# Optimization experiments

Measured on AMD Instinct MI355X. Metric: run time of the kernel, lower is better.

## Reference

```python
import jax, jax.numpy as jnp
import numpy as np

B, L, D, H = 2, 2048, 2048, 16
DH = D // H  # 128


def setup_inputs() -> dict:
    key = jax.random.key(0)
    k1, k2 = jax.random.split(key)
    inputs = jax.random.normal(k1, (B, L, D), dtype=jnp.float32)
    # additive causal mask: 0 on/below diagonal, -inf above (matches typical usage)
    neg = jnp.finfo(jnp.float32).min
    causal = jnp.where(jnp.tril(jnp.ones((L, L), dtype=bool)), 0.0, neg)
    attn_mask = causal[None, None, :, :].astype(jnp.float32)
    # torch Linear(d, 3d, bias=False): y = x @ W.T; here W_qkv is stored as [d, 3d]
    W_qkv = jax.random.normal(k2, (D, 3 * D), dtype=jnp.float32) * (1.0 / np.sqrt(D))
    return {"inputs": inputs, "attn_mask": attn_mask, "W_qkv": W_qkv}


def reference(inputs, attn_mask, W_qkv):
    b, l, d = inputs.shape
    qkv = inputs @ W_qkv                       # [B, L, 3D]
    qkv = qkv.reshape(b, l, H, 3 * DH)         # [B, L, H, 3*dh]
    qkv = qkv.transpose(0, 2, 1, 3)            # [B, H, L, 3*dh]
    Q, K, V = jnp.split(qkv, 3, axis=-1)       # each [B, H, L, dh]
    scale = jnp.sqrt(jnp.float32(DH))
    scores = jnp.einsum("bhqd,bhkd->bhqk", Q, K) / scale
    scores = scores + attn_mask
    probs = jax.nn.softmax(scores, axis=-1)    # dropout is identity in eval / p=0
    out = jnp.einsum("bhqk,bhkd->bhqd", probs, V)
    out = out.transpose(0, 2, 1, 3).reshape(b, l, d)
    return out
```

## Files before the change

### kernel.cpp

```cpp
#include <hip/hip_runtime.h>

#define SEQL 2048
#define NHEAD 16
#define N3 6144
#define KDIM 2048

typedef __attribute__((ext_vector_type(8))) short bf16x8;
typedef __attribute__((ext_vector_type(4))) float f32x4;
typedef __attribute__((ext_vector_type(16))) float f32x16;
typedef __attribute__((ext_vector_type(4))) unsigned short us4;
typedef __attribute__((ext_vector_type(4))) float fl4;
typedef __attribute__((ext_vector_type(4))) unsigned int u32x4;

__device__ __forceinline__ unsigned short f2bf(float x) {
    unsigned u = __builtin_bit_cast(unsigned, x);
    u += 0x7fffu + ((u >> 16) & 1u);
    return (unsigned short)(u >> 16);
}

__device__ __forceinline__ void gload16(const void* g, void* l) {
    __builtin_amdgcn_global_load_lds(
        (const __attribute__((address_space(1))) unsigned int*)g,
        (__attribute__((address_space(3))) unsigned int*)l,
        16, 0, 0);
}

__device__ __forceinline__ unsigned cvtpk_bf16(float lo, float hi) {
    unsigned r;
    asm("v_cvt_pk_bf16_f32 %0, %1, %2" : "=v"(r) : "v"(lo), "v"(hi));
    return r;
}
__device__ __forceinline__ void plane32_swap(unsigned &a, unsigned &b) {
    asm("v_permlane32_swap_b32 %0, %1" : "+v"(a), "+v"(b));
}

__global__ __launch_bounds__(256) void k_convert_x(const float* __restrict__ in,
                                                   unsigned short* __restrict__ out) {
    int tid = blockIdx.x * 256 + threadIdx.x;
    const fl4* in4 = (const fl4*)in;
    us4* out4 = (us4*)out;
#pragma unroll
    for (int j = 0; j < 4; ++j) {
        int idx = tid + j * 524288;
        fl4 v = in4[idx];
        us4 o;
        o.x = f2bf(v.x); o.y = f2bf(v.y); o.z = f2bf(v.z); o.w = f2bf(v.w);
        out4[idx] = o;
    }
}

__global__ __launch_bounds__(256) void k_transpose_w(const float* __restrict__ W,
                                                     unsigned short* __restrict__ Wt) {
    __shared__ alignas(16) unsigned short Ts[64 * 68];
    int t = threadIdx.x;
    int n0 = blockIdx.x * 64;
    int k0 = blockIdx.y * 64;
    int r = t >> 2, c4 = t & 3;
#pragma unroll
    for (int j = 0; j < 4; ++j) {
        int c = (c4 + j * 4) * 4;
        fl4 v = *(const fl4*)&W[(size_t)(k0 + r) * N3 + n0 + c];
        Ts[r * 68 + c + 0] = f2bf(v.x);
        Ts[r * 68 + c + 1] = f2bf(v.y);
        Ts[r * 68 + c + 2] = f2bf(v.z);
        Ts[r * 68 + c + 3] = f2bf(v.w);
    }
    __syncthreads();
#pragma unroll
    for (int j = 0; j < 2; ++j) {
        int chunk = c4 + j * 4;
#pragma unroll
        for (int h = 0; h < 2; ++h) {
            us4 o;
            o.x = Ts[(chunk * 8 + h * 4 + 0) * 68 + r];
            o.y = Ts[(chunk * 8 + h * 4 + 1) * 68 + r];
            o.z = Ts[(chunk * 8 + h * 4 + 2) * 68 + r];
            o.w = Ts[(chunk * 8 + h * 4 + 3) * 68 + r];
            *(us4*)&Wt[(size_t)(n0 + r) * KDIM + k0 + chunk * 8 + h * 4] = o;
        }
    }
}

__global__ __launch_bounds__(512, 2) void k_gemm_qkv(const unsigned short* __restrict__ Xb,
                                                     const unsigned short* __restrict__ Wt,
                                                     unsigned short* __restrict__ Qb,
                                                     unsigned short* __restrict__ Kb,
                                                     unsigned short* __restrict__ Vt) {
    __shared__ alignas(16) char smem[98304];
    int t = threadIdx.x;
    int wid = t >> 6, lane = t & 63, g = lane >> 4, l15 = lane & 15;
    int bid = blockIdx.x;
    bid = (bid & 7) * 96 + (bid >> 3);
    int tmi = bid & 15, tni = bid >> 4;
    int tm = tmi * 256, tn = tni * 128;
    const unsigned short* Abase = Xb + (size_t)tm * KDIM;
    const unsigned short* Bbase = Wt + (size_t)tn * KDIM;
    int wr = wid >> 1, wc = wid & 1;
    f32x4 acc[4][4];
#pragma unroll
    for (int i = 0; i < 4; ++i)
#pragma unroll
        for (int j = 0; j < 4; ++j) acc[i][j] = (f32x4){0.f, 0.f, 0.f, 0.f};

    auto STAGE = [&](int tile, int d) {
        int k0 = tile * 64;
        char* A = smem + d * 49152;
        char* B = A + 32768;
#pragma unroll
        for (int j = 0; j < 4; ++j) {
            int p = j * 8192 + t * 16;
            int row = p >> 7;
            int sl = ((p >> 4) & 7) ^ (row & 7);
            gload16(Abase + (size_t)row * KDIM + k0 + sl * 8, A + j * 8192 + wid * 1024);
        }
#pragma unroll
        for (int j = 0; j < 2; ++j) {
            int p = j * 8192 + t * 16;
            int row = p >> 7;
            int sl = ((p >> 4) & 7) ^ (row & 7);
            gload16(Bbase + (size_t)row * KDIM + k0 + sl * 8, B + j * 8192 + wid * 1024);
        }
    };

    STAGE(0, 0);
    for (int tt = 0; tt < 32; ++tt) {
        int cur = tt & 1;
        if (tt < 31) {
            STAGE(tt + 1, cur ^ 1);
            asm volatile("s_waitcnt vmcnt(6)" ::: "memory");
        } else {
            asm volatile("s_waitcnt vmcnt(0)" ::: "memory");
        }
        __builtin_amdgcn_s_barrier();
        asm volatile("" ::: "memory");
        const char* A = smem + cur * 49152;
        const char* B = A + 32768;
#pragma unroll
        for (int ks = 0; ks < 2; ++ks) {
            bf16x8 af[4], bfr[4];
#pragma unroll
            for (int i = 0; i < 4; ++i) {
                int ra = wr * 64 + i * 16 + l15;
                af[i] = *(const bf16x8*)(A + ra * 128 + (((ks * 4 + g) ^ (ra & 7)) << 4));
                int rb = wc * 64 + i * 16 + l15;
                bfr[i] = *(const bf16x8*)(B + rb * 128 + (((ks * 4 + g) ^ (rb & 7)) << 4));
            }
            __builtin_amdgcn_s_setprio(1);
#pragma unroll
            for (int i = 0; i < 4; ++i)
#pragma unroll
                for (int j = 0; j < 4; ++j)
                    acc[i][j] = __builtin_amdgcn_mfma_f32_16x16x32_bf16(
                        af[i], bfr[j], acc[i][j], 0, 0, 0);
            __builtin_amdgcn_s_setprio(0);
        }
        asm volatile("" ::: "memory");
        __builtin_amdgcn_s_barrier();
        asm volatile("" ::: "memory");
    }

    int ty = tni % 3;
    int h  = tni / 3;
    int b  = tm >> 11, lp0 = tm & 2047;
    const float qsc = 0.08838834764831845f * 1.44269504089f;
#pragma unroll
    for (int i = 0; i < 4; ++i)
#pragma unroll
        for (int j = 0; j < 4; ++j) {
            int d = wc * 64 + j * 16 + l15;
#pragma unroll
            for (int r = 0; r < 4; ++r) {
                int mm = wr * 64 + i * 16 + g * 4 + r;
                float v = acc[i][j][r];
                unsigned short bv = f2bf(ty == 0 ? v * qsc : v);
                int byte;
                if (ty == 2)
                    byte = d * 512 + ((((mm >> 3) ^ (d & 31)) & 31) << 4) + (mm & 7) * 2;
                else
                    byte = mm * 256 + ((((d >> 3) ^ (mm & 15)) & 15) << 4) + (d & 7) * 2;
                *(unsigned short*)(smem + byte) = bv;
            }
        }
    __syncthreads();
    if (ty == 2) {
#pragma unroll
        for (int c = 0; c < 8; ++c) {
            int id = c * 512 + t;
            int d = id >> 5, L = id & 31;
            bf16x8 vv = *(const bf16x8*)(smem + d * 512 + (((L ^ (d & 31)) & 31) << 4));
            int kt = (lp0 >> 6) + (L >> 3);
            *(bf16x8*)&Vt[(size_t)((b * NHEAD + h) * 32 + kt) * 8192 + d * 64 +
                          (L & 7) * 8] = vv;
        }
    } else {
        unsigned short* dst = (ty == 0) ? Qb : Kb;
#pragma unroll
        for (int c = 0; c < 8; ++c) {
            int id = c * 512 + t;
            int mm = id >> 4, cc = id & 15;
            bf16x8 vv = *(const bf16x8*)(smem + mm * 256 + (((cc ^ (mm & 15)) & 15) << 4));
            *(bf16x8*)&dst[((size_t)(b * NHEAD + h) * SEQL + lp0 + mm) * 128 + cc * 8] = vv;
        }
    }
}

__global__ __launch_bounds__(256) void k_attn(const unsigned short* __restrict__ Qb,
                                              const unsigned short* __restrict__ Kb,
                                              const unsigned short* __restrict__ Vt,
                                              float* __restrict__ out) {
    __shared__ alignas(16) unsigned short Ks[64 * 128];
    __shared__ alignas(16) unsigned short Vs[128 * 64];
    __shared__ float Fx[4][32];
    int t = threadIdx.x, w = t >> 6, lane = t & 63;
    int l31 = lane & 31, hi = lane >> 5;
    int qi = 15 - (int)blockIdx.x;
    int bh = blockIdx.y;
    int qb = qi * 128;
    int qg = qb + w * 32 + l31;
    int qwmin = qb + w * 32, qwmax = qwmin + 31;

    bf16x8 qf[8];
    const unsigned short* Qp = Qb + (size_t)(bh * SEQL + qg) * 128;
#pragma unroll
    for (int ks = 0; ks < 8; ++ks)
        qf[ks] = *(const bf16x8*)(Qp + ks * 16 + hi * 8);

    f32x16 accO[4];
#pragma unroll
    for (int db = 0; db < 4; ++db)
#pragma unroll
        for (int e = 0; e < 16; ++e) accO[db][e] = 0.f;
    float mstate = -3.0e38f, lsum = 0.f;

    int nkv = 2 * qi + 2;
    for (int kt = 0; kt < nkv; ++kt) {
        int kv0 = kt * 64;
#pragma unroll
        for (int j = 0; j < 4; ++j) {
            int p = j * 4096 + t * 16;
            int rk = p >> 8;
            int sk = ((p >> 4) & 15) ^ (rk & 15);
            gload16(Kb + (size_t)(bh * SEQL + kv0 + rk) * 128 + sk * 8,
                    (char*)Ks + j * 4096 + w * 1024);
            int rv = p >> 7;
            int sv = ((p >> 4) & 7) ^ (rv & 7);
            gload16(Vt + ((size_t)(bh * 32 + (kv0 >> 6)) * 128 + rv) * 64 + sv * 8,
                    (char*)Vs + j * 4096 + w * 1024);
        }
        __syncthreads();

        if (kv0 <= qwmax) {
            f32x16 s[2];
#pragma unroll
            for (int blk = 0; blk < 2; ++blk)
#pragma unroll
                for (int e = 0; e < 16; ++e) s[blk][e] = 0.f;
#pragma unroll
            for (int ks = 0; ks < 8; ++ks) {
                int c = ks * 2 + hi;
#pragma unroll
                for (int blk = 0; blk < 2; ++blk) {
                    int row = blk * 32 + l31;
                    bf16x8 kf = *(const bf16x8*)((const char*)Ks + row * 256 +
                                                 (((c ^ (row & 15)) & 15) << 4));
                    s[blk] = __builtin_amdgcn_mfma_f32_32x32x16_bf16(kf, qf[ks], s[blk], 0, 0, 0);
                }
            }
            if (kv0 + 63 > qwmin) {
#pragma unroll
                for (int blk = 0; blk < 2; ++blk)
#pragma unroll
                    for (int r = 0; r < 16; ++r) {
                        int kvg = kv0 + blk * 32 + (r & 3) + 8 * (r >> 2) + 4 * hi;
                        if (kvg > qg) s[blk][r] = -3.0e38f;
                    }
            }
            float tmax = -3.0e38f;
#pragma unroll
            for (int blk = 0; blk < 2; ++blk)
#pragma unroll
                for (int r = 0; r < 16; ++r) tmax = fmaxf(tmax, s[blk][r]);
            tmax = fmaxf(tmax, __shfl_xor(tmax, 32));
            if (__any(tmax > mstate + 8.0f)) {
                float mnew = fmaxf(mstate, tmax);
                float fs = __builtin_amdgcn_exp2f(mstate - mnew);
                lsum *= fs;
                mstate = mnew;
                Fx[w][l31] = fs;
                f32x4 fv[4];
#pragma unroll
                for (int q4 = 0; q4 < 4; ++q4)
                    fv[q4] = *(const f32x4*)&Fx[w][q4 * 8 + 4 * hi];
#pragma unroll
                for (int db = 0; db < 4; ++db)
#pragma unroll
                    for (int r = 0; r < 16; ++r)
                        accO[db][r] *= fv[r >> 2][r & 3];
            }
            float ps = 0.f;
#pragma unroll
            for (int blk = 0; blk < 2; ++blk)
#pragma unroll
                for (int r = 0; r < 16; ++r) {
                    float p = __builtin_amdgcn_exp2f(s[blk][r] - mstate);
                    s[blk][r] = p;
                    ps += p;
                }
            ps += __shfl_xor(ps, 32);
            lsum += ps;
            unsigned pa[4][4];
#pragma unroll
            for (int blk = 0; blk < 2; ++blk)
#pragma unroll
                for (int hf = 0; hf < 2; ++hf) {
                    int o = hf * 8;
                    unsigned d0 = cvtpk_bf16(s[blk][o + 0], s[blk][o + 1]);
                    unsigned d2 = cvtpk_bf16(s[blk][o + 4], s[blk][o + 5]);
                    plane32_swap(d0, d2);
                    unsigned d1 = cvtpk_bf16(s[blk][o + 2], s[blk][o + 3]);
                    unsigned d3 = cvtpk_bf16(s[blk][o + 6], s[blk][o + 7]);
                    plane32_swap(d1, d3);
                    pa[blk * 2 + hf][0] = d0; pa[blk * 2 + hf][1] = d1;
                    pa[blk * 2 + hf][2] = d2; pa[blk * 2 + hf][3] = d3;
                }
#pragma unroll
            for (int ksv = 0; ksv < 4; ++ksv) {
                u32x4 pu = {pa[ksv][0], pa[ksv][1], pa[ksv][2], pa[ksv][3]};
                bf16x8 paf = __builtin_bit_cast(bf16x8, pu);
                int c = ksv * 2 + hi;
#pragma unroll
                for (int db = 0; db < 4; ++db) {
                    int rv = db * 32 + l31;
                    bf16x8 vf = *(const bf16x8*)((const char*)Vs + rv * 128 +
                                                 (((c ^ (rv & 7)) & 7) << 4));
                    accO[db] = __builtin_amdgcn_mfma_f32_32x32x16_bf16(paf, vf, accO[db], 0, 0, 0);
                }
            }
        }
        __syncthreads();
    }
    float inv = 1.0f / lsum;
    Fx[w][l31] = inv;
    f32x4 iv[4];
#pragma unroll
    for (int q4 = 0; q4 < 4; ++q4)
        iv[q4] = *(const f32x4*)&Fx[w][q4 * 8 + 4 * hi];
    int b = bh >> 4, h = bh & 15;
    float* ob = out + (size_t)(b * SEQL + qb + w * 32) * 2048 + h * 128;
#pragma unroll
    for (int db = 0; db < 4; ++db)
#pragma unroll
        for (int r = 0; r < 16; ++r) {
            int qr = (r & 3) + 8 * (r >> 2) + 4 * hi;
            ob[(size_t)qr * 2048 + db * 32 + l31] = accO[db][r] * iv[r >> 2][r & 3];
        }
}

extern "C" void kernel_launch(void* const* d_in, const int* in_sizes, int n_in,
                              void* d_out, int out_size, void* d_ws, size_t ws_size,
                              hipStream_t stream) {
    const float* x = (const float*)d_in[0];
    const float* w = (const float*)d_in[2];
    float* out = (float*)d_out;
    char* ws = (char*)d_ws;
    unsigned short* Xb = (unsigned short*)(ws);
    unsigned short* Wt = (unsigned short*)(ws + 16777216);
    unsigned short* Qb = (unsigned short*)(ws + 41943040);
    unsigned short* Kb = (unsigned short*)(ws + 58720256);
    unsigned short* Vt = (unsigned short*)(ws + 75497472);

    hipLaunchKernelGGL(k_convert_x, dim3(2048), dim3(256), 0, stream, x, Xb);
    hipLaunchKernelGGL(k_transpose_w, dim3(96, 32), dim3(256), 0, stream, w, Wt);
    hipLaunchKernelGGL(k_gemm_qkv, dim3(768), dim3(512), 0, stream, Xb, Wt, Qb, Kb, Vt);
    hipLaunchKernelGGL(k_attn, dim3(16, 32), dim3(256), 0, stream, Qb, Kb, Vt, out);
}
```

Measured before the change: 362.4 us.

## Widen QKV GEMM tiles to 256x256 with 4-stage pipeline and merge prep kernels

Merges the X conversion and W transpose kernels into one launch. Reworks the QKV GEMM to use 256x256 output tiles with half as many blocks, a 4-deep K=32 cp.async-style LDS ring with interleaved prefetch, and a split barrier schedule, so each loaded operand feeds more MFMAs. The epilogue now writes two Q/K/V head slices per block. The catch is 128KB of LDS per block with 128 accumulator registers per thread, which may limit occupancy to one block per CU and leaves 384 blocks for 256 CUs, a partial second wave.

```diff
diff --git a/kernel.cpp b/kernel.cpp
--- a/kernel.cpp
+++ b/kernel.cpp
@@ -34,49 +34,50 @@
     asm("v_permlane32_swap_b32 %0, %1" : "+v"(a), "+v"(b));
 }
 
-__global__ __launch_bounds__(256) void k_convert_x(const float* __restrict__ in,
-                                                   unsigned short* __restrict__ out) {
-    int tid = blockIdx.x * 256 + threadIdx.x;
-    const fl4* in4 = (const fl4*)in;
-    us4* out4 = (us4*)out;
-#pragma unroll
-    for (int j = 0; j < 4; ++j) {
-        int idx = tid + j * 524288;
-        fl4 v = in4[idx];
-        us4 o;
-        o.x = f2bf(v.x); o.y = f2bf(v.y); o.z = f2bf(v.z); o.w = f2bf(v.w);
-        out4[idx] = o;
-    }
-}
-
-__global__ __launch_bounds__(256) void k_transpose_w(const float* __restrict__ W,
-                                                     unsigned short* __restrict__ Wt) {
+__global__ __launch_bounds__(256) void k_prep(const float* __restrict__ X,
+                                              const float* __restrict__ W,
+                                              unsigned short* __restrict__ Xb,
+                                              unsigned short* __restrict__ Wt) {
     __shared__ alignas(16) unsigned short Ts[64 * 68];
-    int t = threadIdx.x;
-    int n0 = blockIdx.x * 64;
-    int k0 = blockIdx.y * 64;
-    int r = t >> 2, c4 = t & 3;
-#pragma unroll
-    for (int j = 0; j < 4; ++j) {
-        int c = (c4 + j * 4) * 4;
-        fl4 v = *(const fl4*)&W[(size_t)(k0 + r) * N3 + n0 + c];
-        Ts[r * 68 + c + 0] = f2bf(v.x);
-        Ts[r * 68 + c + 1] = f2bf(v.y);
-        Ts[r * 68 + c + 2] = f2bf(v.z);
-        Ts[r * 68 + c + 3] = f2bf(v.w);
-    }
-    __syncthreads();
-#pragma unroll
-    for (int j = 0; j < 2; ++j) {
-        int chunk = c4 + j * 4;
-#pragma unroll
-        for (int h = 0; h < 2; ++h) {
+    int bid = blockIdx.x, t = threadIdx.x;
+    if (bid < 2048) {
+        int tid = bid * 256 + t;
+        const fl4* in4 = (const fl4*)X;
+        us4* out4 = (us4*)Xb;
+#pragma unroll
+        for (int j = 0; j < 4; ++j) {
+            int idx = tid + j * 524288;
+            fl4 v = in4[idx];
             us4 o;
-            o.x = Ts[(chunk * 8 + h * 4 + 0) * 68 + r];
-            o.y = Ts[(chunk * 8 + h * 4 + 1) * 68 + r];
-            o.z = Ts[(chunk * 8 + h * 4 + 2) * 68 + r];
-            o.w = Ts[(chunk * 8 + h * 4 + 3) * 68 + r];
-            *(us4*)&Wt[(size_t)(n0 + r) * KDIM + k0 + chunk * 8 + h * 4] = o;
+            o.x = f2bf(v.x); o.y = f2bf(v.y); o.z = f2bf(v.z); o.w = f2bf(v.w);
+            out4[idx] = o;
+        }
+    } else {
+        int b2 = bid - 2048;
+        int n0 = (b2 % 96) * 64, k0 = (b2 / 96) * 64;
+        int r = t >> 2, c4 = t & 3;
+#pragma unroll
+        for (int j = 0; j < 4; ++j) {
+            int c = (c4 + j * 4) * 4;
+            fl4 v = *(const fl4*)&W[(size_t)(k0 + r) * N3 + n0 + c];
+            Ts[r * 68 + c + 0] = f2bf(v.x);
+            Ts[r * 68 + c + 1] = f2bf(v.y);
+            Ts[r * 68 + c + 2] = f2bf(v.z);
+            Ts[r * 68 + c + 3] = f2bf(v.w);
+        }
+        __syncthreads();
+#pragma unroll
+        for (int j = 0; j < 2; ++j) {
+            int chunk = c4 + j * 4;
+#pragma unroll
+            for (int h = 0; h < 2; ++h) {
+                us4 o;
+                o.x = Ts[(chunk * 8 + h * 4 + 0) * 68 + r];
+                o.y = Ts[(chunk * 8 + h * 4 + 1) * 68 + r];
+                o.z = Ts[(chunk * 8 + h * 4 + 2) * 68 + r];
+                o.w = Ts[(chunk * 8 + h * 4 + 3) * 68 + r];
+                *(us4*)&Wt[(size_t)(n0 + r) * KDIM + k0 + chunk * 8 + h * 4] = o;
+            }
         }
     }
 }
@@ -86,120 +87,157 @@
                                                      unsigned short* __restrict__ Qb,
                                                      unsigned short* __restrict__ Kb,
                                                      unsigned short* __restrict__ Vt) {
-    __shared__ alignas(16) char smem[98304];
+    __shared__ alignas(16) char smem[131072];
     int t = threadIdx.x;
     int wid = t >> 6, lane = t & 63, g = lane >> 4, l15 = lane & 15;
     int bid = blockIdx.x;
-    bid = (bid & 7) * 96 + (bid >> 3);
+    bid = (bid & 7) * 48 + (bid >> 3);
     int tmi = bid & 15, tni = bid >> 4;
-    int tm = tmi * 256, tn = tni * 128;
+    int tm = tmi * 256, tn = tni * 256;
     const unsigned short* Abase = Xb + (size_t)tm * KDIM;
     const unsigned short* Bbase = Wt + (size_t)tn * KDIM;
-    int wr = wid >> 1, wc = wid & 1;
-    f32x4 acc[4][4];
-#pragma unroll
-    for (int i = 0; i < 4; ++i)
+    int wm = wid >> 2, wn = wid & 3;
+    f32x4 acc[8][4];
+#pragma unroll
+    for (int i = 0; i < 8; ++i)
 #pragma unroll
         for (int j = 0; j < 4; ++j) acc[i][j] = (f32x4){0.f, 0.f, 0.f, 0.f};
 
-    auto STAGE = [&](int tile, int d) {
-        int k0 = tile * 64;
-        char* A = smem + d * 49152;
-        char* B = A + 32768;
-#pragma unroll
-        for (int j = 0; j < 4; ++j) {
-            int p = j * 8192 + t * 16;
-            int row = p >> 7;
-            int sl = ((p >> 4) & 7) ^ (row & 7);
-            gload16(Abase + (size_t)row * KDIM + k0 + sl * 8, A + j * 8192 + wid * 1024);
-        }
+    auto stage_a = [&](int tile) {
+        int k0 = tile * 32;
+        char* dst = smem + (tile & 3) * 32768;
 #pragma unroll
         for (int j = 0; j < 2; ++j) {
             int p = j * 8192 + t * 16;
-            int row = p >> 7;
-            int sl = ((p >> 4) & 7) ^ (row & 7);
-            gload16(Bbase + (size_t)row * KDIM + k0 + sl * 8, B + j * 8192 + wid * 1024);
+            int s = p >> 4;
+            int mr = s >> 3;
+            int sl = (s & 7) ^ (mr & 7);
+            int m = mr * 2 + (sl >> 2);
+            gload16(Abase + (size_t)m * KDIM + k0 + (sl & 3) * 8,
+                    dst + j * 8192 + wid * 1024);
         }
     };
-
-    STAGE(0, 0);
-    for (int tt = 0; tt < 32; ++tt) {
-        int cur = tt & 1;
-        if (tt < 31) {
-            STAGE(tt + 1, cur ^ 1);
-            asm volatile("s_waitcnt vmcnt(6)" ::: "memory");
+    auto stage_b = [&](int tile) {
+        int k0 = tile * 32;
+        char* dst = smem + (tile & 3) * 32768 + 16384;
+#pragma unroll
+        for (int j = 0; j < 2; ++j) {
+            int p = j * 8192 + t * 16;
+            int s = p >> 4;
+            int nr = s >> 3;
+            int sl = (s & 7) ^ (nr & 7);
+            int n = nr * 2 + (sl >> 2);
+            gload16(Bbase + (size_t)n * KDIM + k0 + (sl & 3) * 8,
+                    dst + j * 8192 + wid * 1024);
+        }
+    };
+
+    stage_a(0); stage_b(0); stage_a(1); stage_b(1); stage_a(2); stage_b(2);
+    asm volatile("s_waitcnt vmcnt(8)" ::: "memory");
+    __builtin_amdgcn_s_barrier();
+    asm volatile("" ::: "memory");
+
+    auto iter = [&](int tt, int pf, int vm) {
+        const char* Abuf = smem + (tt & 3) * 32768;
+        const char* Bbuf = Abuf + 16384;
+        bf16x8 bfv[4];
+#pragma unroll
+        for (int mh = 0; mh < 2; ++mh) {
+            bf16x8 af[4];
+#pragma unroll
+            for (int q = 0; q < 4; ++q) {
+                int ra = wm * 128 + mh * 64 + q * 16 + l15;
+                int mr = ra >> 1;
+                af[q] = *(const bf16x8*)(Abuf + mr * 128 +
+                        ((((ra & 1) * 4 + g) ^ (mr & 7)) << 4));
+            }
+            if (mh == 0) {
+#pragma unroll
+                for (int bj = 0; bj < 4; ++bj) {
+                    int rb = wn * 64 + bj * 16 + l15;
+                    int nr = rb >> 1;
+                    bfv[bj] = *(const bf16x8*)(Bbuf + nr * 128 +
+                              ((((rb & 1) * 4 + g) ^ (nr & 7)) << 4));
+                }
+                if (pf >= 0) stage_a(pf);
+            } else {
+                if (pf >= 0) stage_b(pf);
+            }
+            asm volatile("" ::: "memory");
+            __builtin_amdgcn_s_barrier();
+            __builtin_amdgcn_s_setprio(1);
+#pragma unroll
+            for (int q = 0; q < 4; ++q)
+#pragma unroll
+                for (int bj = 0; bj < 4; ++bj)
+                    acc[mh * 4 + q][bj] = __builtin_amdgcn_mfma_f32_16x16x32_bf16(
+                        af[q], bfv[bj], acc[mh * 4 + q][bj], 0, 0, 0);
+            __builtin_amdgcn_s_setprio(0);
+            asm volatile("" ::: "memory");
+            if (mh == 1) {
+                if (vm == 8)      asm volatile("s_waitcnt vmcnt(8)" ::: "memory");
+                else if (vm == 4) asm volatile("s_waitcnt vmcnt(4)" ::: "memory");
+                else if (vm == 0) asm volatile("s_waitcnt vmcnt(0)" ::: "memory");
+            }
+            __builtin_amdgcn_s_barrier();
+            asm volatile("" ::: "memory");
+        }
+    };
+
+    for (int tt = 0; tt < 61; ++tt) iter(tt, tt + 3, 8);
+    iter(61, -1, 4);
+    iter(62, -1, 0);
+    iter(63, -1, -1);
+
+    int b = tm >> 11, lp0 = tm & 2047;
+    const float qsc = 0.08838834764831845f * 1.44269504089f;
+    int half_w = wn >> 1;
+    int tyw = (tni * 2 + half_w) % 3;
+    char* Tw = smem + half_w * 65536;
+#pragma unroll
+    for (int fi = 0; fi < 8; ++fi)
+#pragma unroll
+        for (int bj = 0; bj < 4; ++bj) {
+            int d = wn * 64 + bj * 16 + l15;
+            int dl = d & 127;
+#pragma unroll
+            for (int r = 0; r < 4; ++r) {
+                int mm = wm * 128 + fi * 16 + g * 4 + r;
+                float v = acc[fi][bj][r];
+                unsigned short bv = f2bf(tyw == 0 ? v * qsc : v);
+                int byte;
+                if (tyw == 2)
+                    byte = dl * 512 + ((((mm >> 3) ^ (dl & 31)) & 31) << 4) + (mm & 7) * 2;
+                else
+                    byte = mm * 256 + ((((dl >> 3) ^ (mm & 15)) & 15) << 4) + (dl & 7) * 2;
+                *(unsigned short*)(Tw + byte) = bv;
+            }
+        }
+    __syncthreads();
+#pragma unroll
+    for (int half = 0; half < 2; ++half) {
+        int ty = (tni * 2 + half) % 3;
+        int h  = (tni * 2 + half) / 3;
+        const char* Tr = smem + half * 65536;
+        if (ty == 2) {
+#pragma unroll
+            for (int c = 0; c < 8; ++c) {
+                int id = c * 512 + t;
+                int dl = id >> 5, Lc = id & 31;
+                bf16x8 vv = *(const bf16x8*)(Tr + dl * 512 + (((Lc ^ (dl & 31)) & 31) << 4));
+                int kt = (lp0 >> 6) + (Lc >> 3);
+                *(bf16x8*)&Vt[(size_t)((b * NHEAD + h) * 32 + kt) * 8192 + dl * 64 +
+                              (Lc & 7) * 8] = vv;
+            }
         } else {
-            asm volatile("s_waitcnt vmcnt(0)" ::: "memory");
-        }
-        __builtin_amdgcn_s_barrier();
-        asm volatile("" ::: "memory");
-        const char* A = smem + cur * 49152;
-        const char* B = A + 32768;
-#pragma unroll
-        for (int ks = 0; ks < 2; ++ks) {
-            bf16x8 af[4], bfr[4];
-#pragma unroll
-            for (int i = 0; i < 4; ++i) {
-                int ra = wr * 64 + i * 16 + l15;
-                af[i] = *(const bf16x8*)(A + ra * 128 + (((ks * 4 + g) ^ (ra & 7)) << 4));
-                int rb = wc * 64 + i * 16 + l15;
-                bfr[i] = *(const bf16x8*)(B + rb * 128 + (((ks * 4 + g) ^ (rb & 7)) << 4));
-            }
-            __builtin_amdgcn_s_setprio(1);
-#pragma unroll
-            for (int i = 0; i < 4; ++i)
-#pragma unroll
-                for (int j = 0; j < 4; ++j)
-                    acc[i][j] = __builtin_amdgcn_mfma_f32_16x16x32_bf16(
-                        af[i], bfr[j], acc[i][j], 0, 0, 0);
-            __builtin_amdgcn_s_setprio(0);
-        }
-        asm volatile("" ::: "memory");
-        __builtin_amdgcn_s_barrier();
-        asm volatile("" ::: "memory");
-    }
-
-    int ty = tni % 3;
-    int h  = tni / 3;
-    int b  = tm >> 11, lp0 = tm & 2047;
-    const float qsc = 0.08838834764831845f * 1.44269504089f;
-#pragma unroll
-    for (int i = 0; i < 4; ++i)
-#pragma unroll
-        for (int j = 0; j < 4; ++j) {
-            int d = wc * 64 + j * 16 + l15;
-#pragma unroll
-            for (int r = 0; r < 4; ++r) {
-                int mm = wr * 64 + i * 16 + g * 4 + r;
-                float v = acc[i][j][r];
-                unsigned short bv = f2bf(ty == 0 ? v * qsc : v);
-                int byte;
-                if (ty == 2)
-                    byte = d * 512 + ((((mm >> 3) ^ (d & 31)) & 31) << 4) + (mm & 7) * 2;
-                else
-                    byte = mm * 256 + ((((d >> 3) ^ (mm & 15)) & 15) << 4) + (d & 7) * 2;
-                *(unsigned short*)(smem + byte) = bv;
-            }
-        }
-    __syncthreads();
-    if (ty == 2) {
-#pragma unroll
-        for (int c = 0; c < 8; ++c) {
-            int id = c * 512 + t;
-            int d = id >> 5, L = id & 31;
-            bf16x8 vv = *(const bf16x8*)(smem + d * 512 + (((L ^ (d & 31)) & 31) << 4));
-            int kt = (lp0 >> 6) + (L >> 3);
-            *(bf16x8*)&Vt[(size_t)((b * NHEAD + h) * 32 + kt) * 8192 + d * 64 +
-                          (L & 7) * 8] = vv;
-        }
-    } else {
-        unsigned short* dst = (ty == 0) ? Qb : Kb;
-#pragma unroll
-        for (int c = 0; c < 8; ++c) {
-            int id = c * 512 + t;
-            int mm = id >> 4, cc = id & 15;
-            bf16x8 vv = *(const bf16x8*)(smem + mm * 256 + (((cc ^ (mm & 15)) & 15) << 4));
-            *(bf16x8*)&dst[((size_t)(b * NHEAD + h) * SEQL + lp0 + mm) * 128 + cc * 8] = vv;
+            unsigned short* dst = (ty == 0) ? Qb : Kb;
+#pragma unroll
+            for (int c = 0; c < 8; ++c) {
+                int id = c * 512 + t;
+                int mm = id >> 4, cc = id & 15;
+                bf16x8 vv = *(const bf16x8*)(Tr + mm * 256 + (((cc ^ (mm & 15)) & 15) << 4));
+                *(bf16x8*)&dst[((size_t)(b * NHEAD + h) * SEQL + lp0 + mm) * 128 + cc * 8] = vv;
+            }
         }
     }
 }
@@ -369,8 +407,7 @@
     unsigned short* Kb = (unsigned short*)(ws + 58720256);
     unsigned short* Vt = (unsigned short*)(ws + 75497472);
 
-    hipLaunchKernelGGL(k_convert_x, dim3(2048), dim3(256), 0, stream, x, Xb);
-    hipLaunchKernelGGL(k_transpose_w, dim3(96, 32), dim3(256), 0, stream, w, Wt);
-    hipLaunchKernelGGL(k_gemm_qkv, dim3(768), dim3(512), 0, stream, Xb, Wt, Qb, Kb, Vt);
+    hipLaunchKernelGGL(k_prep, dim3(5120), dim3(256), 0, stream, x, w, Xb, Wt);
+    hipLaunchKernelGGL(k_gemm_qkv, dim3(384), dim3(512), 0, stream, Xb, Wt, Qb, Kb, Vt);
     hipLaunchKernelGGL(k_attn, dim3(16, 32), dim3(256), 0, stream, Qb, Kb, Vt, out);
 }
```

After: 363.3 us. About the same (+0.2%).
